# Kernel optimization log

Hardware: AMD Instinct MI355X
Metric: run time of the kernel (lower is better)

## Reference

```python
import jax, jax.numpy as jnp
import numpy as np

N, E, EDGES, G = 4096, 256, 131072, 64
H, DH = 4, 64  # MHA heads, head dim


def _ln(x, g, b, eps=1e-5):
    m = jnp.mean(x, -1, keepdims=True)
    v = jnp.var(x, -1, keepdims=True)
    return g * (x - m) * jax.lax.rsqrt(v + eps) + b


def setup_inputs() -> dict:
    key = jax.random.key(0)
    ks = jax.random.split(key, 40)
    i = iter(range(40))
    def rn(shape, s=1.0):
        return jax.random.normal(ks[next(i)], shape, jnp.float32) * s
    w = lambda shape: rn(shape, 0.02)
    inp = {
        "node_hidden": rn((N, E)),
        "edge_hidden": rn((EDGES, E)),
        "pos": rn((N, 3)),
        # GINEConv MLP: Lin(E,2E) -> LN -> ReLU -> Dropout -> Lin(2E,E)
        "gine_w1": w((E, 2 * E)), "gine_b1": jnp.zeros((2 * E,)),
        "gine_ln_g": jnp.ones((2 * E,)), "gine_ln_b": jnp.zeros((2 * E,)),
        "gine_w2": w((2 * E, E)), "gine_b2": jnp.zeros((E,)),
        "norm1_g": jnp.ones((E,)), "norm1_b": jnp.zeros((E,)),
        # DirectionalMessagePassing params
        "dir_w": w((3, E)), "dir_b": jnp.zeros((E,)),
        "msg_w": w((E, E)), "msg_b": jnp.zeros((E,)),
        # MultiheadAttention
        "wq": w((E, E)), "bq": jnp.zeros((E,)),
        "wk": w((E, E)), "bk": jnp.zeros((E,)),
        "wv": w((E, E)), "bv": jnp.zeros((E,)),
        "wo": w((E, E)), "bo": jnp.zeros((E,)),
        # gate
        "gate_w": w((2 * E, E)), "gate_b": jnp.zeros((E,)),
        "norm2_g": jnp.ones((E,)), "norm2_b": jnp.zeros((E,)),
        # GraphNorm affine
        "gn_g": jnp.ones((E,)), "gn_b": jnp.zeros((E,)),
        # int inputs
        "edge_index": jax.random.randint(ks[next(i)], (2, EDGES), 0, N, jnp.int64 if jax.config.jax_enable_x64 else jnp.int32),
        "node_id": jnp.sort(jax.random.randint(ks[next(i)], (N,), 0, G)),
        "edge_id": jax.random.randint(ks[next(i)], (EDGES,), 0, G),
    }
    return inp


def reference(node_hidden, edge_hidden, pos,
              gine_w1, gine_b1, gine_ln_g, gine_ln_b, gine_w2, gine_b2,
              norm1_g, norm1_b, dir_w, dir_b, msg_w, msg_b,
              wq, bq, wk, bk, wv, bv, wo, bo,
              gate_w, gate_b, norm2_g, norm2_b, gn_g, gn_b,
              edge_index, node_id, edge_id):
    src, dst = edge_index[0], edge_index[1]
    identity = node_hidden

    # --- GINEConv: out = MLP(x + sum_j relu(x_j + e_ij)), eps=0 ---
    msg = jax.nn.relu(node_hidden[src] + edge_hidden)           # [EDGES, E]
    agg = jax.ops.segment_sum(msg, dst, num_segments=N)         # [N, E]
    h = node_hidden + agg
    h = jax.nn.relu(_ln(h @ gine_w1 + gine_b1, gine_ln_g, gine_ln_b))
    gnn_out = _ln(h @ gine_w2 + gine_b2, norm1_g, norm1_b)      # norm1

    # --- DirectionalMessagePassing over unit edge directions ---
    vec = pos[dst] - pos[src]                                   # [EDGES, 3]
    vec = vec / (jnp.linalg.norm(vec, axis=-1, keepdims=True) + 1e-8)
    dfeat = vec @ dir_w + dir_b                                 # [EDGES, E]
    smsg = gnn_out[src] * dfeat
    sagg = jax.ops.segment_sum(smsg, dst, num_segments=N)
    spatial_out = sagg @ msg_w + msg_b                          # [N, E]

    # --- MHA: q = gnn_out, k = v = spatial_out (seq = nodes, batch=1) ---
    q = (gnn_out @ wq + bq).reshape(N, H, DH)
    k = (spatial_out @ wk + bk).reshape(N, H, DH)
    v = (spatial_out @ wv + bv).reshape(N, H, DH)
    scores = jnp.einsum("nhd,mhd->hnm", q, k) / np.sqrt(DH)
    attn = jax.nn.softmax(scores, axis=-1)
    fused = jnp.einsum("hnm,mhd->nhd", attn, v).reshape(N, E) @ wo + bo

    # --- gated residual blend + norm2 ---
    gate = jax.nn.sigmoid(jnp.concatenate([fused, identity], -1) @ gate_w + gate_b)
    out = gate * fused + (1.0 - gate) * identity
    out = _ln(out, norm2_g, norm2_b)

    # --- GraphNorm: per-graph mean/var over nodes (segment stats) ---
    counts = jax.ops.segment_sum(jnp.ones((N, 1), out.dtype), node_id, num_segments=G)
    mean = jax.ops.segment_sum(out, node_id, num_segments=G) / counts
    cen = out - mean[node_id]
    var = jax.ops.segment_sum(cen * cen, node_id, num_segments=G) / counts
    out = gn_g * cen * jax.lax.rsqrt(var[node_id] + 1e-5) + gn_b

    # last_act = True; dropout is eval-mode identity
    return jax.nn.relu(out)
```

## Files before the change

### kernel.cpp

```cpp
#include <hip/hip_runtime.h>
#include <hip/hip_bf16.h>

#define N_NODES 4096
#define E_DIM   256
#define N_EDGES 131072
#define N_GRAPHS 64
#define H_HEADS 4
#define DH      64
#define SPLIT   4

typedef unsigned short u16;
typedef __attribute__((ext_vector_type(8))) short bf16x8;
typedef __attribute__((ext_vector_type(4))) float f32x4;

__device__ __forceinline__ float u2f(u16 u) {
    union { unsigned int i; float f; } c; c.i = ((unsigned int)u) << 16; return c.f;
}
__device__ __forceinline__ u16 f2bu(float f) {
    __hip_bfloat16 h = __float2bfloat16(f);
    return *reinterpret_cast<u16*>(&h);
}
__device__ __forceinline__ float ldv(const void* p, size_t i, int f32) {
    return f32 ? ((const float*)p)[i] : u2f(((const u16*)p)[i]);
}
__device__ __forceinline__ float4 ldv4(const void* p, size_t i, int f32) {
    if (f32) return *(const float4*)((const float*)p + i);
    ushort4 u = *(const ushort4*)((const u16*)p + i);
    return make_float4(u2f(u.x), u2f(u.y), u2f(u.z), u2f(u.w));
}
__device__ __forceinline__ int ldi(const int* p, int i, int i64) {
    return i64 ? p[2 * i] : p[i];
}

__global__ void k_detect(const u16* __restrict__ ones_raw, const int* __restrict__ ei_raw,
                         int* __restrict__ flags) {
    flags[0] = (ones_raw[0] == 0) ? 1 : 0;
    flags[1] = (ei_raw[1] == 0 && ei_raw[3] == 0 && ei_raw[5] == 0 && ei_raw[7] == 0) ? 1 : 0;
}

__global__ void k_cvt(const void* __restrict__ s, float* __restrict__ d, int n,
                      const int* __restrict__ flags) {
    int i = blockIdx.x * 256 + threadIdx.x;
    if (i < n) d[i] = ldv(s, i, flags[0]);
}

struct SmDesc { const void* src; float* dst; int n; };
struct SmTable { SmDesc d[19]; };
__global__ __launch_bounds__(256) void k_cvts(SmTable tb, const int* __restrict__ flags) {
    int ti = blockIdx.x / 48;
    int off = (blockIdx.x % 48) * 256 + threadIdx.x;
    SmDesc e = tb.d[ti];
    if (off < e.n) e.dst[off] = ldv(e.src, off, flags[0]);
}

struct WtDesc { const void* src; u16* dst; int K; int N; int base; };
struct WtTable { WtDesc d[8]; };
__global__ __launch_bounds__(256) void k_cvtw(WtTable tb, const int* __restrict__ flags) {
    __shared__ u16 tile[64][68];
    int b = blockIdx.x;
    int i = 0;
    while (i < 7 && b >= tb.d[i + 1].base) i++;
    WtDesc e = tb.d[i];
    int tl = b - e.base;
    int ntn = e.N >> 6;
    int kt = tl / ntn, nt = tl % ntn;
    int t = threadIdx.x, r = t >> 2, c0 = (t & 3) * 16;
    int f32 = flags[0];
#pragma unroll
    for (int j = 0; j < 16; j++)
        tile[r][c0 + j] = f2bu(ldv(e.src, (size_t)(kt * 64 + r) * e.N + nt * 64 + c0 + j, f32));
    __syncthreads();
#pragma unroll
    for (int j = 0; j < 16; j++)
        e.dst[(size_t)(nt * 64 + r) * e.K + kt * 64 + c0 + j] = tile[c0 + j][r];
}

__global__ __launch_bounds__(256) void k_mgemm(const float* __restrict__ A0, const float* __restrict__ A1,
                                               int K0, int Ktot, const u16* __restrict__ BT,
                                               const float* __restrict__ bias, void* __restrict__ C,
                                               int Nc, int outbf) {
    __shared__ u16 As[64 * 64];
    __shared__ u16 Bs[64 * 64];
    int t = threadIdx.x;
    int wv = t >> 6, l = t & 63, lg = l >> 4, lc = l & 15;
    int wm = wv >> 1, wn = wv & 1;
    int m0 = blockIdx.y * 64, n0 = blockIdx.x * 64;
    f32x4 acc[2][2] = {};
    int sr = t >> 2, sc = (t & 3) * 16;
    int sw = (sr & 7) << 3;

    for (int k0 = 0; k0 < Ktot; k0 += 64) {
        const float* Ap = (k0 < K0) ? (A0 + (size_t)(m0 + sr) * K0 + k0 + sc)
                                    : (A1 + (size_t)(m0 + sr) * (Ktot - K0) + (k0 - K0) + sc);
#pragma unroll
        for (int j = 0; j < 2; j++) {
            float4 f0 = *(const float4*)(Ap + j * 8);
            float4 f1 = *(const float4*)(Ap + j * 8 + 4);
            bf16x8 bv;
            bv[0] = (short)f2bu(f0.x); bv[1] = (short)f2bu(f0.y);
            bv[2] = (short)f2bu(f0.z); bv[3] = (short)f2bu(f0.w);
            bv[4] = (short)f2bu(f1.x); bv[5] = (short)f2bu(f1.y);
            bv[6] = (short)f2bu(f1.z); bv[7] = (short)f2bu(f1.w);
            *(bf16x8*)&As[(sr * 64 + sc + j * 8) ^ sw] = bv;
        }
        const u16* Bp = BT + (size_t)(n0 + sr) * Ktot + k0 + sc;
        *(bf16x8*)&Bs[(sr * 64 + sc) ^ sw]     = *(const bf16x8*)Bp;
        *(bf16x8*)&Bs[(sr * 64 + sc + 8) ^ sw] = *(const bf16x8*)(Bp + 8);
        __syncthreads();
#pragma unroll
        for (int ks = 0; ks < 2; ks++) {
            bf16x8 af[2], bfr[2];
#pragma unroll
            for (int mi = 0; mi < 2; mi++) {
                int row = wm * 32 + mi * 16 + lc;
                af[mi] = *(const bf16x8*)&As[(row * 64 + ks * 32 + lg * 8) ^ ((row & 7) << 3)];
            }
#pragma unroll
            for (int ni = 0; ni < 2; ni++) {
                int col = wn * 32 + ni * 16 + lc;
                bfr[ni] = *(const bf16x8*)&Bs[(col * 64 + ks * 32 + lg * 8) ^ ((col & 7) << 3)];
            }
#pragma unroll
            for (int mi = 0; mi < 2; mi++)
#pragma unroll
                for (int ni = 0; ni < 2; ni++)
                    acc[mi][ni] = __builtin_amdgcn_mfma_f32_16x16x32_bf16(af[mi], bfr[ni], acc[mi][ni], 0, 0, 0);
        }
        __syncthreads();
    }
#pragma unroll
    for (int mi = 0; mi < 2; mi++)
#pragma unroll
        for (int ni = 0; ni < 2; ni++) {
            int col = n0 + wn * 32 + ni * 16 + lc;
            float bb = bias ? bias[col] : 0.f;
#pragma unroll
            for (int r = 0; r < 4; r++) {
                int row = m0 + wm * 32 + mi * 16 + lg * 4 + r;
                float v = acc[mi][ni][r] + bb;
                if (outbf) ((u16*)C)[(size_t)row * Nc + col] = f2bu(v);
                else       ((float*)C)[(size_t)row * Nc + col] = v;
            }
        }
}

__global__ __launch_bounds__(256) void k_transV(const u16* __restrict__ KVh, u16* __restrict__ VT) {
    __shared__ u16 tile[64][72];
    int n0 = blockIdx.x * 64, h = blockIdx.y, t = threadIdx.x;
    int r = t >> 2, c0 = (t & 3) * 16;
    const u16* src = &KVh[(size_t)(n0 + r) * 512 + 256 + h * DH + c0];
    *(bf16x8*)&tile[r][c0]     = *(const bf16x8*)src;
    *(bf16x8*)&tile[r][c0 + 8] = *(const bf16x8*)(src + 8);
    __syncthreads();
    u16* dst = &VT[((size_t)h * DH + r) * N_NODES + n0 + c0];
#pragma unroll
    for (int j = 0; j < 16; j++) dst[j] = tile[c0 + j][r];
}

__global__ __launch_bounds__(256) void k_attn(const u16* __restrict__ Qh, const u16* __restrict__ KVh,
                                              const u16* __restrict__ VT, u16* __restrict__ part) {
    __shared__ u16 K_lds[64 * 64];
    __shared__ u16 V_lds[64 * 64];
    __shared__ u16 P_lds[4][16 * 64];
    int t = threadIdx.x;
    int wv = t >> 6, l = t & 63;
    int lg = l >> 4, lc = l & 15;
    int h = blockIdx.y, c = blockIdx.z;
    int q0 = blockIdx.x * 64 + wv * 16;

    bf16x8 qf[2];
#pragma unroll
    for (int kk = 0; kk < 2; kk++)
        qf[kk] = *(const bf16x8*)&Qh[(size_t)(q0 + lc) * E_DIM + h * DH + kk * 32 + lg * 8];

    f32x4 oacc[4] = {};
    float mrow[4], lrow[4];
#pragma unroll
    for (int r = 0; r < 4; r++) { mrow[r] = -1e30f; lrow[r] = 0.f; }

    int lr = t >> 2, lc16 = (t & 3) * 16;

    for (int kv0 = c * (N_NODES / SPLIT); kv0 < (c + 1) * (N_NODES / SPLIT); kv0 += 64) {
        __syncthreads();
        {
            int base = lr * 64 + lc16;
            int sw = (lr & 7) << 3;
            const u16* kp = &KVh[(size_t)(kv0 + lr) * 512 + h * DH + lc16];
            *(bf16x8*)&K_lds[(base) ^ sw]     = *(const bf16x8*)kp;
            *(bf16x8*)&K_lds[(base + 8) ^ sw] = *(const bf16x8*)(kp + 8);
            const u16* vp = &VT[((size_t)h * DH + lr) * N_NODES + kv0 + lc16];
            *(bf16x8*)&V_lds[(base) ^ sw]     = *(const bf16x8*)vp;
            *(bf16x8*)&V_lds[(base + 8) ^ sw] = *(const bf16x8*)(vp + 8);
        }
        __syncthreads();

        f32x4 s[4];
#pragma unroll
        for (int n = 0; n < 4; n++) {
            f32x4 a = {};
#pragma unroll
            for (int kk = 0; kk < 2; kk++) {
                int row = n * 16 + lc;
                bf16x8 b = *(const bf16x8*)&K_lds[(row * 64 + kk * 32 + lg * 8) ^ ((row & 7) << 3)];
                a = __builtin_amdgcn_mfma_f32_16x16x32_bf16(qf[kk], b, a, 0, 0, 0);
            }
            s[n] = a;
        }
        float tm[4];
#pragma unroll
        for (int r = 0; r < 4; r++) {
#pragma unroll
            for (int n = 0; n < 4; n++) s[n][r] *= 0.125f;
            tm[r] = fmaxf(fmaxf(s[0][r], s[1][r]), fmaxf(s[2][r], s[3][r]));
        }
#pragma unroll
        for (int msk = 1; msk < 16; msk <<= 1)
#pragma unroll
            for (int r = 0; r < 4; r++) tm[r] = fmaxf(tm[r], __shfl_xor(tm[r], msk));

        float p[4][4], psum[4];
#pragma unroll
        for (int r = 0; r < 4; r++) {
            float nm = fmaxf(mrow[r], tm[r]);
            float alpha = __expf(mrow[r] - nm);
            lrow[r] *= alpha;
#pragma unroll
            for (int n = 0; n < 4; n++) oacc[n][r] *= alpha;
            float ps = 0.f;
#pragma unroll
            for (int n = 0; n < 4; n++) { p[n][r] = __expf(s[n][r] - nm); ps += p[n][r]; }
            psum[r] = ps;
            mrow[r] = nm;
        }
#pragma unroll
        for (int msk = 1; msk < 16; msk <<= 1)
#pragma unroll
            for (int r = 0; r < 4; r++) psum[r] += __shfl_xor(psum[r], msk);
#pragma unroll
        for (int r = 0; r < 4; r++) lrow[r] += psum[r];

#pragma unroll
        for (int r = 0; r < 4; r++) {
            int q = lg * 4 + r;
            int sw = (q & 7) << 3;
#pragma unroll
            for (int n = 0; n < 4; n++)
                P_lds[wv][(q * 64 + n * 16 + lc) ^ sw] = f2bu(p[n][r]);
        }
#pragma unroll
        for (int kc = 0; kc < 2; kc++) {
            bf16x8 a = *(const bf16x8*)&P_lds[wv][(lc * 64 + kc * 32 + lg * 8) ^ ((lc & 7) << 3)];
#pragma unroll
            for (int n = 0; n < 4; n++) {
                int row = n * 16 + lc;
                bf16x8 b = *(const bf16x8*)&V_lds[(row * 64 + kc * 32 + lg * 8) ^ ((row & 7) << 3)];
                oacc[n] = __builtin_amdgcn_mfma_f32_16x16x32_bf16(a, b, oacc[n], 0, 0, 0);
            }
        }
    }

#pragma unroll
    for (int r = 0; r < 4; r++) {
        u16* pp = part + ((size_t)(c * H_HEADS + h) * N_NODES + q0 + lg * 4 + r) * 72;
#pragma unroll
        for (int n = 0; n < 4; n++) pp[n * 16 + lc] = f2bu(oacc[n][r]);
        if (lc == 0) { *(float*)(pp + 64) = mrow[r]; *(float*)(pp + 66) = lrow[r]; }
    }
}

__global__ __launch_bounds__(256) void k_combine(const u16* __restrict__ part, float* __restrict__ attno) {
    int n = blockIdx.x, t = threadIdx.x;
    int h = t >> 6, d = t & 63;
    float M = -1e30f;
#pragma unroll
    for (int c = 0; c < SPLIT; c++)
        M = fmaxf(M, *(const float*)(part + ((size_t)(c * H_HEADS + h) * N_NODES + n) * 72 + 64));
    float L = 0.f, o = 0.f;
#pragma unroll
    for (int c = 0; c < SPLIT; c++) {
        const u16* pp = part + ((size_t)(c * H_HEADS + h) * N_NODES + n) * 72;
        float w = __expf(*(const float*)(pp + 64) - M);
        L = fmaf(*(const float*)(pp + 66), w, L);
        o = fmaf(u2f(pp[d]), w, o);
    }
    attno[(size_t)n * E_DIM + h * DH + d] = o / L;
}

__device__ __forceinline__ void block_red2(float& a, float& b, float* sbuf) {
#pragma unroll
    for (int o = 32; o > 0; o >>= 1) { a += __shfl_down(a, o); b += __shfl_down(b, o); }
    int w = threadIdx.x >> 6;
    if ((threadIdx.x & 63) == 0) { sbuf[w] = a; sbuf[4 + w] = b; }
    __syncthreads();
    a = sbuf[0] + sbuf[1] + sbuf[2] + sbuf[3];
    b = sbuf[4] + sbuf[5] + sbuf[6] + sbuf[7];
    __syncthreads();
}

__global__ void k_count(const int* __restrict__ ei, int* __restrict__ count,
                        const int* __restrict__ flags) {
    int e = blockIdx.x * 256 + threadIdx.x;
    int i64 = flags[1];
    int d = i64 ? ei[2 * (N_EDGES + e)] : ei[N_EDGES + e];
    atomicAdd(&count[d], 1);
}

__global__ __launch_bounds__(1024) void k_scan(const int* __restrict__ count,
                                               int* __restrict__ offs, int* __restrict__ cursor) {
    __shared__ int s[1024];
    int t = threadIdx.x;
    int c0 = count[t * 4 + 0], c1 = count[t * 4 + 1], c2 = count[t * 4 + 2], c3 = count[t * 4 + 3];
    int tot = c0 + c1 + c2 + c3;
    s[t] = tot; __syncthreads();
    for (int o = 1; o < 1024; o <<= 1) {
        int v = (t >= o) ? s[t - o] : 0;
        __syncthreads();
        s[t] += v;
        __syncthreads();
    }
    int base = (t > 0) ? s[t - 1] : 0;
    int o0 = base, o1 = base + c0, o2 = o1 + c1, o3 = o2 + c2;
    offs[t * 4 + 0] = o0; offs[t * 4 + 1] = o1; offs[t * 4 + 2] = o2; offs[t * 4 + 3] = o3;
    cursor[t * 4 + 0] = o0; cursor[t * 4 + 1] = o1; cursor[t * 4 + 2] = o2; cursor[t * 4 + 3] = o3;
    if (t == 1023) offs[4096] = s[1023];
}

__global__ void k_scatter(const int* __restrict__ ei, int* __restrict__ cursor,
                          int* __restrict__ elist, const int* __restrict__ flags) {
    int e = blockIdx.x * 256 + threadIdx.x;
    int i64 = flags[1];
    int d = i64 ? ei[2 * (N_EDGES + e)] : ei[N_EDGES + e];
    int p = atomicAdd(&cursor[d], 1);
    elist[p] = e;
}

__global__ __launch_bounds__(256) void k_gine_agg(const float* __restrict__ xf, const void* __restrict__ eh,
                                                  const int* __restrict__ ei, const int* __restrict__ offs,
                                                  const int* __restrict__ elist, const int* __restrict__ flags,
                                                  float* __restrict__ hout) {
    int wv = threadIdx.x >> 6, ld = threadIdx.x & 63;
    int n = blockIdx.x * 4 + wv;
    int f32 = flags[0], i64 = flags[1];
    int cc = ld * 4;
    float4 acc = *(const float4*)&xf[(size_t)n * E_DIM + cc];
    int i0 = offs[n], i1 = offs[n + 1];
    int i = i0;
    for (; i + 2 <= i1; i += 2) {
        int e0 = elist[i], e1 = elist[i + 1];
        int s0 = ldi(ei, e0, i64), s1 = ldi(ei, e1, i64);
        float4 a0 = ldv4(eh, (size_t)e0 * E_DIM + cc, f32);
        float4 x0 = *(const float4*)&xf[(size_t)s0 * E_DIM + cc];
        float4 a1 = ldv4(eh, (size_t)e1 * E_DIM + cc, f32);
        float4 x1 = *(const float4*)&xf[(size_t)s1 * E_DIM + cc];
        acc.x += fmaxf(x0.x + a0.x, 0.f) + fmaxf(x1.x + a1.x, 0.f);
        acc.y += fmaxf(x0.y + a0.y, 0.f) + fmaxf(x1.y + a1.y, 0.f);
        acc.z += fmaxf(x0.z + a0.z, 0.f) + fmaxf(x1.z + a1.z, 0.f);
        acc.w += fmaxf(x0.w + a0.w, 0.f) + fmaxf(x1.w + a1.w, 0.f);
    }
    if (i < i1) {
        int e0 = elist[i];
        int s0 = ldi(ei, e0, i64);
        float4 a0 = ldv4(eh, (size_t)e0 * E_DIM + cc, f32);
        float4 x0 = *(const float4*)&xf[(size_t)s0 * E_DIM + cc];
        acc.x += fmaxf(x0.x + a0.x, 0.f);
        acc.y += fmaxf(x0.y + a0.y, 0.f);
        acc.z += fmaxf(x0.z + a0.z, 0.f);
        acc.w += fmaxf(x0.w + a0.w, 0.f);
    }
    *(float4*)&hout[(size_t)n * E_DIM + cc] = acc;
}

template <int W>
__global__ __launch_bounds__(256) void k_ln(float* __restrict__ X, const float* __restrict__ g,
                                            const float* __restrict__ b, int relu) {
    __shared__ float sbuf[8];
    constexpr int PE = W / 256;
    int n = blockIdx.x, t = threadIdx.x;
    float* row = X + (size_t)n * W;
    float x[PE];
    float s = 0.f, s2 = 0.f;
#pragma unroll
    for (int i = 0; i < PE; i++) { x[i] = row[t + i * 256]; s += x[i]; s2 += x[i] * x[i]; }
    block_red2(s, s2, sbuf);
    float mean = s / W;
    float var = fmaxf(s2 / W - mean * mean, 0.f);
    float rstd = rsqrtf(var + 1e-5f);
#pragma unroll
    for (int i = 0; i < PE; i++) {
        int c = t + i * 256;
        float y = g[c] * (x[i] - mean) * rstd + b[c];
        if (relu) y = fmaxf(y, 0.f);
        row[c] = y;
    }
}

__global__ __launch_bounds__(256) void k_dir(const float* __restrict__ posf, const int* __restrict__ ei,
                                             const int* __restrict__ offs, const int* __restrict__ elist,
                                             const int* __restrict__ flags,
                                             const float* __restrict__ gnn, const float* __restrict__ dw,
                                             const float* __restrict__ db, float* __restrict__ sagg) {
    int wv = threadIdx.x >> 6, ld = threadIdx.x & 63;
    int n = blockIdx.x * 4 + wv;
    int i64 = flags[1];
    int cc = ld * 4;
    float4 w0 = *(const float4*)&dw[cc];
    float4 w1 = *(const float4*)&dw[256 + cc];
    float4 w2 = *(const float4*)&dw[512 + cc];
    float4 bb = *(const float4*)&db[cc];
    float px = posf[n * 3 + 0], py = posf[n * 3 + 1], pz = posf[n * 3 + 2];
    float4 acc = {0.f, 0.f, 0.f, 0.f};
    int i0 = offs[n], i1 = offs[n + 1];
    int i = i0;
    for (; i + 2 <= i1; i += 2) {
        int e0 = elist[i], e1 = elist[i + 1];
        int s0 = ldi(ei, e0, i64), s1 = ldi(ei, e1, i64);
        float q0x = posf[s0 * 3 + 0], q0y = posf[s0 * 3 + 1], q0z = posf[s0 * 3 + 2];
        float q1x = posf[s1 * 3 + 0], q1y = posf[s1 * 3 + 1], q1z = posf[s1 * 3 + 2];
        float4 g0 = *(const float4*)&gnn[(size_t)s0 * E_DIM + cc];
        float4 g1 = *(const float4*)&gnn[(size_t)s1 * E_DIM + cc];
        float vx0 = px - q0x, vy0 = py - q0y, vz0 = pz - q0z;
        float vx1 = px - q1x, vy1 = py - q1y, vz1 = pz - q1z;
        float rn0 = 1.f / (sqrtf(vx0 * vx0 + vy0 * vy0 + vz0 * vz0) + 1e-8f);
        float rn1 = 1.f / (sqrtf(vx1 * vx1 + vy1 * vy1 + vz1 * vz1) + 1e-8f);
        acc.x = fmaf(g0.x, bb.x + (vx0 * w0.x + vy0 * w1.x + vz0 * w2.x) * rn0, acc.x);
        acc.y = fmaf(g0.y, bb.y + (vx0 * w0.y + vy0 * w1.y + vz0 * w2.y) * rn0, acc.y);
        acc.z = fmaf(g0.z, bb.z + (vx0 * w0.z + vy0 * w1.z + vz0 * w2.z) * rn0, acc.z);
        acc.w = fmaf(g0.w, bb.w + (vx0 * w0.w + vy0 * w1.w + vz0 * w2.w) * rn0, acc.w);
        acc.x = fmaf(g1.x, bb.x + (vx1 * w0.x + vy1 * w1.x + vz1 * w2.x) * rn1, acc.x);
        acc.y = fmaf(g1.y, bb.y + (vx1 * w0.y + vy1 * w1.y + vz1 * w2.y) * rn1, acc.y);
        acc.z = fmaf(g1.z, bb.z + (vx1 * w0.z + vy1 * w1.z + vz1 * w2.z) * rn1, acc.z);
        acc.w = fmaf(g1.w, bb.w + (vx1 * w0.w + vy1 * w1.w + vz1 * w2.w) * rn1, acc.w);
    }
    if (i < i1) {
        int e0 = elist[i];
        int s0 = ldi(ei, e0, i64);
        float q0x = posf[s0 * 3 + 0], q0y = posf[s0 * 3 + 1], q0z = posf[s0 * 3 + 2];
        float4 g0 = *(const float4*)&gnn[(size_t)s0 * E_DIM + cc];
        float vx0 = px - q0x, vy0 = py - q0y, vz0 = pz - q0z;
        float rn0 = 1.f / (sqrtf(vx0 * vx0 + vy0 * vy0 + vz0 * vz0) + 1e-8f);
        acc.x = fmaf(g0.x, bb.x + (vx0 * w0.x + vy0 * w1.x + vz0 * w2.x) * rn0, acc.x);
        acc.y = fmaf(g0.y, bb.y + (vx0 * w0.y + vy0 * w1.y + vz0 * w2.y) * rn0, acc.y);
        acc.z = fmaf(g0.z, bb.z + (vx0 * w0.z + vy0 * w1.z + vz0 * w2.z) * rn0, acc.z);
        acc.w = fmaf(g0.w, bb.w + (vx0 * w0.w + vy0 * w1.w + vz0 * w2.w) * rn0, acc.w);
    }
    *(float4*)&sagg[(size_t)n * E_DIM + cc] = acc;
}

__global__ __launch_bounds__(256) void k_gate_ln(const float* __restrict__ gl, const float* __restrict__ fused,
                                                 const float* __restrict__ xf, const float* __restrict__ g2,
                                                 const float* __restrict__ b2, float* __restrict__ out2) {
    __shared__ float sbuf[8];
    int n = blockIdx.x, t = threadIdx.x;
    float z = gl[(size_t)n * E_DIM + t];
    float gate = 1.f / (1.f + __expf(-z));
    float o = gate * fused[(size_t)n * E_DIM + t] + (1.f - gate) * xf[(size_t)n * E_DIM + t];
    float s = o, s2 = o * o;
    block_red2(s, s2, sbuf);
    float mean = s / E_DIM;
    float var = fmaxf(s2 / E_DIM - mean * mean, 0.f);
    float y = g2[t] * (o - mean) * rsqrtf(var + 1e-5f) + b2[t];
    out2[(size_t)n * E_DIM + t] = y;
}

__global__ void k_bounds(const int* __restrict__ nid, int* __restrict__ startg,
                         const int* __restrict__ flags) {
    int t = threadIdx.x;
    int i64 = flags[1];
    if (t <= N_GRAPHS) {
        int lo = 0, hi = N_NODES;
        while (lo < hi) { int mid = (lo + hi) >> 1; if (ldi(nid, mid, i64) < t) lo = mid + 1; else hi = mid; }
        startg[t] = lo;
    }
}

__global__ __launch_bounds__(256) void k_gnstats(const int* __restrict__ startg, const float* __restrict__ out2,
                                                 float* __restrict__ gnm, float* __restrict__ gnr) {
    int g = blockIdx.x, t = threadIdx.x;
    int a = startg[g], bnd = startg[g + 1];
    int cnt = bnd - a;
    float s = 0.f, s2 = 0.f;
    for (int n = a; n < bnd; n++) {
        float x = out2[(size_t)n * E_DIM + t];
        s += x; s2 = fmaf(x, x, s2);
    }
    float inv = cnt ? 1.f / (float)cnt : 0.f;
    float mean = s * inv;
    float var = fmaxf(s2 * inv - mean * mean, 0.f);
    gnm[g * E_DIM + t] = mean;
    gnr[g * E_DIM + t] = rsqrtf(var + 1e-5f);
}

__global__ __launch_bounds__(256) void k_gnapply(const float* __restrict__ out2, const int* __restrict__ nid,
                                                 const float* __restrict__ gnm, const float* __restrict__ gnr,
                                                 const float* __restrict__ gg, const float* __restrict__ gb,
                                                 const int* __restrict__ flags, void* __restrict__ out) {
    int n = blockIdx.x, t = threadIdx.x;
    int g = ldi(nid, n, flags[1]);
    float y = gg[t] * (out2[(size_t)n * E_DIM + t] - gnm[g * E_DIM + t]) * gnr[g * E_DIM + t] + gb[t];
    y = fmaxf(y, 0.f);
    size_t idx = (size_t)n * E_DIM + t;
    if (flags[0]) ((float*)out)[idx] = y;
    else ((__hip_bfloat16*)out)[idx] = __float2bfloat16(y);
}

extern "C" void kernel_launch(void* const* d_in, const int* in_sizes, int n_in,
                              void* d_out, int out_size, void* d_ws, size_t ws_size,
                              hipStream_t stream) {
    const void* x_r    = d_in[0];
    const void* eh_r   = d_in[1];
    const void* pos_r  = d_in[2];
    const void* w1_r   = d_in[3];
    const void* b1_r   = d_in[4];
    const void* glng_r = d_in[5];
    const void* glnb_r = d_in[6];
    const void* w2_r   = d_in[7];
    const void* b2_r   = d_in[8];
    const void* n1g_r  = d_in[9];
    const void* n1b_r  = d_in[10];
    const void* dirw_r = d_in[11];
    const void* dirb_r = d_in[12];
    const void* msgw_r = d_in[13];
    const void* msgb_r = d_in[14];
    const void* wq_r   = d_in[15];
    const void* bq_r   = d_in[16];
    const void* wk_r   = d_in[17];
    const void* bk_r   = d_in[18];
    const void* wv_r   = d_in[19];
    const void* bv_r   = d_in[20];
    const void* wo_r   = d_in[21];
    const void* bo_r   = d_in[22];
    const void* gw_r   = d_in[23];
    const void* gb_r   = d_in[24];
    const void* n2g_r  = d_in[25];
    const void* n2b_r  = d_in[26];
    const void* gng_r  = d_in[27];
    const void* gnb_r  = d_in[28];
    const int* ei      = (const int*)d_in[29];
    const int* nid     = (const int*)d_in[30];

    char* ws = (char*)d_ws;
    const size_t KB = 1 << 10, MB = 1 << 20;
    int*   flags  = (int*)(ws + 0);
    int*   count  = (int*)(ws + 16 * KB);
    int*   offs   = (int*)(ws + 32 * KB);
    int*   cursor = (int*)(ws + 64 * KB);
    int*   elist  = (int*)(ws + 128 * KB);

    float* posf   = (float*)(ws + 1 * MB);
    float* prm    = (float*)(ws + 1 * MB + 64 * KB);
    float* b1f   = prm + 0;
    float* glngf = prm + 512,  *glnbf = prm + 1024;
    float* b2f   = prm + 1536;
    float* n1gf  = prm + 1792, *n1bf  = prm + 2048;
    float* dirwf = prm + 2304;
    float* dirbf = prm + 3072, *msgbf = prm + 3328;
    float* bqf   = prm + 3584, *bkf   = prm + 3840, *bvf = prm + 4096, *bof = prm + 4352;
    float* gbf   = prm + 4608;
    float* n2gf  = prm + 4864, *n2bf  = prm + 5120;
    float* gngf  = prm + 5376, *gnbf  = prm + 5632;

    u16* w1t   = (u16*)(ws + 2 * MB);
    u16* w2t   = (u16*)(ws + 2 * MB + 256 * KB);
    u16* msgwt = (u16*)(ws + 2 * MB + 512 * KB);
    u16* wqt   = (u16*)(ws + 2 * MB + 640 * KB);
    u16* wkvt  = (u16*)(ws + 2 * MB + 768 * KB);
    u16* wot   = (u16*)(ws + 3 * MB + 0 * KB);
    u16* gwt   = (u16*)(ws + 3 * MB + 128 * KB);

    float* xf     = (float*)(ws + 5 * MB);
    float* hbuf   = (float*)(ws + 9 * MB);
    float* T1     = (float*)(ws + 13 * MB);
    float* gnn    = (float*)(ws + 21 * MB);
    float* sagg   = (float*)(ws + 25 * MB);
    float* spat   = (float*)(ws + 29 * MB);
    u16*   Qh     = (u16*)(ws + 9 * MB);
    u16*   KVh    = (u16*)(ws + 13 * MB);
    u16*   VT     = (u16*)(ws + 17 * MB);
    u16*   part   = (u16*)(ws + 19 * MB);
    float* attno  = (float*)(ws + 13 * MB);
    float* fused  = (float*)(ws + 29 * MB);
    float* gatel  = (float*)(ws + 19 * MB);
    float* out2   = (float*)(ws + 23 * MB);
    float* gnm    = (float*)(ws + 29 * MB);
    float* gnr    = (float*)(ws + 29 * MB + 64 * KB);
    int*   startg = (int*)(ws + 29 * MB + 128 * KB);

    k_detect<<<1, 1, 0, stream>>>((const u16*)glng_r, ei, flags);

    k_cvt<<<(N_NODES * E_DIM + 255) / 256, 256, 0, stream>>>(x_r, xf, N_NODES * E_DIM, flags);

    SmTable st;
    {
        int i = 0;
        auto add = [&](const void* s, float* d, int n) { st.d[i].src = s; st.d[i].dst = d; st.d[i].n = n; i++; };
        add(pos_r, posf, N_NODES * 3);
        add(b1_r, b1f, 512); add(glng_r, glngf, 512); add(glnb_r, glnbf, 512);
        add(b2_r, b2f, 256); add(n1g_r, n1gf, 256); add(n1b_r, n1bf, 256);
        add(dirw_r, dirwf, 768); add(dirb_r, dirbf, 256); add(msgb_r, msgbf, 256);
        add(bq_r, bqf, 256); add(bk_r, bkf, 256); add(bv_r, bvf, 256); add(bo_r, bof, 256);
        add(gb_r, gbf, 256); add(n2g_r, n2gf, 256); add(n2b_r, n2bf, 256);
        add(gng_r, gngf, 256); add(gnb_r, gnbf, 256);
    }
    k_cvts<<<19 * 48, 256, 0, stream>>>(st, flags);

    WtTable wt;
    {
        int i = 0, base = 0;
        auto add = [&](const void* s, u16* d, int K, int N) {
            wt.d[i].src = s; wt.d[i].dst = d; wt.d[i].K = K; wt.d[i].N = N; wt.d[i].base = base;
            base += (K / 64) * (N / 64); i++;
        };
        add(w1_r, w1t, 256, 512);
        add(w2_r, w2t, 512, 256);
        add(msgw_r, msgwt, 256, 256);
        add(wq_r, wqt, 256, 256);
        add(wk_r, wkvt, 256, 256);
        add(wv_r, wkvt + 256 * 256, 256, 256);
        add(wo_r, wot, 256, 256);
        add(gw_r, gwt, 512, 256);
        k_cvtw<<<base, 256, 0, stream>>>(wt, flags);
    }

    hipMemsetAsync(count, 0, N_NODES * sizeof(int), stream);
    k_count<<<N_EDGES / 256, 256, 0, stream>>>(ei, count, flags);
    k_scan<<<1, 1024, 0, stream>>>(count, offs, cursor);
    k_scatter<<<N_EDGES / 256, 256, 0, stream>>>(ei, cursor, elist, flags);

    k_gine_agg<<<N_NODES / 4, 256, 0, stream>>>(xf, eh_r, ei, offs, elist, flags, hbuf);
    k_mgemm<<<dim3(8, 64), 256, 0, stream>>>(hbuf, nullptr, 256, 256, w1t, b1f, T1, 512, 0);
    k_ln<512><<<N_NODES, 256, 0, stream>>>(T1, glngf, glnbf, 1);
    k_mgemm<<<dim3(4, 64), 256, 0, stream>>>(T1, nullptr, 512, 512, w2t, b2f, gnn, 256, 0);
    k_ln<256><<<N_NODES, 256, 0, stream>>>(gnn, n1gf, n1bf, 0);

    k_dir<<<N_NODES / 4, 256, 0, stream>>>(posf, ei, offs, elist, flags, gnn, dirwf, dirbf, sagg);
    k_mgemm<<<dim3(4, 64), 256, 0, stream>>>(sagg, nullptr, 256, 256, msgwt, msgbf, spat, 256, 0);

    k_mgemm<<<dim3(4, 64), 256, 0, stream>>>(gnn, nullptr, 256, 256, wqt, bqf, Qh, 256, 1);
    k_mgemm<<<dim3(8, 64), 256, 0, stream>>>(spat, nullptr, 256, 256, wkvt, bkf, KVh, 512, 1);
    k_transV<<<dim3(64, 4), 256, 0, stream>>>(KVh, VT);

    k_attn<<<dim3(N_NODES / 64, H_HEADS, SPLIT), 256, 0, stream>>>(Qh, KVh, VT, part);
    k_combine<<<N_NODES, 256, 0, stream>>>(part, attno);
    k_mgemm<<<dim3(4, 64), 256, 0, stream>>>(attno, nullptr, 256, 256, wot, bof, fused, 256, 0);

    k_mgemm<<<dim3(4, 64), 256, 0, stream>>>(fused, xf, 256, 512, gwt, gbf, gatel, 256, 0);
    k_gate_ln<<<N_NODES, 256, 0, stream>>>(gatel, fused, xf, n2gf, n2bf, out2);

    k_bounds<<<1, 128, 0, stream>>>(nid, startg, flags);
    k_gnstats<<<N_GRAPHS, 256, 0, stream>>>(startg, out2, gnm, gnr);
    k_gnapply<<<N_NODES, 256, 0, stream>>>(out2, nid, gnm, gnr, gngf, gnbf, flags, d_out);
}
```

Baseline: 295.6 us.

## Fold msg projection into K/V weights and fuse QKV GEMM with V transpose

Precomputes msg_w·[wk|wv] and the matching biases so spatial_out is never materialised, then computes Q, K and V in a single GEMM over [gnn|sagg] that also writes the transposed V directly. It also doubles the attention KV split, writes the attention output as bf16 so the out-projection reads bf16, replaces the 1024-thread scan with a wave-shuffle scan, unrolls the GINE gather by four, and folds the graph-bound search into the stats kernel. This removes several kernel launches and intermediate buffers. The price is extra per-call weight-prep GEMMs, and multiplying the weights together before rounding to bf16 changes the rounding behaviour.

Measured after the change: 292.2 us. Within noise of the previous version (-1.1%).

```diff
diff --git a/kernel.cpp b/kernel.cpp
--- a/kernel.cpp
+++ b/kernel.cpp
@@ -7,7 +7,7 @@
 #define N_GRAPHS 64
 #define H_HEADS 4
 #define DH      64
-#define SPLIT   4
+#define SPLIT   8
 
 typedef unsigned short u16;
 typedef __attribute__((ext_vector_type(8))) short bf16x8;
@@ -42,6 +42,17 @@
                       const int* __restrict__ flags) {
     int i = blockIdx.x * 256 + threadIdx.x;
     if (i < n) d[i] = ldv(s, i, flags[0]);
+}
+
+__global__ void k_cvtb(const void* __restrict__ s, u16* __restrict__ d, int n4,
+                       const int* __restrict__ flags) {
+    int i = blockIdx.x * 256 + threadIdx.x;
+    if (i < n4) {
+        float4 v = ldv4(s, (size_t)i * 4, flags[0]);
+        ushort4 o;
+        o.x = f2bu(v.x); o.y = f2bu(v.y); o.z = f2bu(v.z); o.w = f2bu(v.w);
+        ((ushort4*)d)[i] = o;
+    }
 }
 
 struct SmDesc { const void* src; float* dst; int n; };
@@ -75,10 +86,24 @@
         e.dst[(size_t)(nt * 64 + r) * e.K + kt * 64 + c0 + j] = tile[c0 + j][r];
 }
 
-__global__ __launch_bounds__(256) void k_mgemm(const float* __restrict__ A0, const float* __restrict__ A1,
+__global__ __launch_bounds__(256) void k_biasfold(const float* __restrict__ bq, const float* __restrict__ bk,
+                                                  const float* __restrict__ bv, const float* __restrict__ msgb,
+                                                  const u16* __restrict__ wkvt, float* __restrict__ bqkv) {
+    int t = blockIdx.x * 256 + threadIdx.x;
+    if (t < 256) { bqkv[t] = bq[t]; return; }
+    int c = t - 256;
+    float s = (c < 256) ? bk[c] : bv[c - 256];
+    const u16* row = wkvt + (size_t)c * 256;
+    float acc = 0.f;
+    for (int k = 0; k < 256; k++) acc = fmaf(msgb[k], u2f(row[k]), acc);
+    bqkv[256 + c] = s + acc;
+}
+
+__global__ __launch_bounds__(256) void k_mgemm(const void* __restrict__ A0, const void* __restrict__ A1,
                                                int K0, int Ktot, const u16* __restrict__ BT,
                                                const float* __restrict__ bias, void* __restrict__ C,
-                                               int Nc, int outbf) {
+                                               int Nc, int outbf, int abf, int mode,
+                                               u16* __restrict__ vt) {
     __shared__ u16 As[64 * 64];
     __shared__ u16 Bs[64 * 64];
     int t = threadIdx.x;
@@ -90,18 +115,27 @@
     int sw = (sr & 7) << 3;
 
     for (int k0 = 0; k0 < Ktot; k0 += 64) {
-        const float* Ap = (k0 < K0) ? (A0 + (size_t)(m0 + sr) * K0 + k0 + sc)
-                                    : (A1 + (size_t)(m0 + sr) * (Ktot - K0) + (k0 - K0) + sc);
-#pragma unroll
-        for (int j = 0; j < 2; j++) {
-            float4 f0 = *(const float4*)(Ap + j * 8);
-            float4 f1 = *(const float4*)(Ap + j * 8 + 4);
-            bf16x8 bv;
-            bv[0] = (short)f2bu(f0.x); bv[1] = (short)f2bu(f0.y);
-            bv[2] = (short)f2bu(f0.z); bv[3] = (short)f2bu(f0.w);
-            bv[4] = (short)f2bu(f1.x); bv[5] = (short)f2bu(f1.y);
-            bv[6] = (short)f2bu(f1.z); bv[7] = (short)f2bu(f1.w);
-            *(bf16x8*)&As[(sr * 64 + sc + j * 8) ^ sw] = bv;
+        const void* Abase; int astride, kof;
+        if (mode == 1) { Abase = (n0 < K0) ? A0 : A1; astride = Ktot; kof = k0; }
+        else if (k0 < K0) { Abase = A0; astride = K0; kof = k0; }
+        else { Abase = A1; astride = Ktot - K0; kof = k0 - K0; }
+        if (abf) {
+            const u16* Ap = (const u16*)Abase + (size_t)(m0 + sr) * astride + kof + sc;
+            *(bf16x8*)&As[(sr * 64 + sc) ^ sw]     = *(const bf16x8*)Ap;
+            *(bf16x8*)&As[(sr * 64 + sc + 8) ^ sw] = *(const bf16x8*)(Ap + 8);
+        } else {
+            const float* Ap = (const float*)Abase + (size_t)(m0 + sr) * astride + kof + sc;
+#pragma unroll
+            for (int j = 0; j < 2; j++) {
+                float4 f0 = *(const float4*)(Ap + j * 8);
+                float4 f1 = *(const float4*)(Ap + j * 8 + 4);
+                bf16x8 bv;
+                bv[0] = (short)f2bu(f0.x); bv[1] = (short)f2bu(f0.y);
+                bv[2] = (short)f2bu(f0.z); bv[3] = (short)f2bu(f0.w);
+                bv[4] = (short)f2bu(f1.x); bv[5] = (short)f2bu(f1.y);
+                bv[6] = (short)f2bu(f1.z); bv[7] = (short)f2bu(f1.w);
+                *(bf16x8*)&As[(sr * 64 + sc + j * 8) ^ sw] = bv;
+            }
         }
         const u16* Bp = BT + (size_t)(n0 + sr) * Ktot + k0 + sc;
         *(bf16x8*)&Bs[(sr * 64 + sc) ^ sw]     = *(const bf16x8*)Bp;
@@ -138,27 +172,16 @@
             for (int r = 0; r < 4; r++) {
                 int row = m0 + wm * 32 + mi * 16 + lg * 4 + r;
                 float v = acc[mi][ni][r] + bb;
-                if (outbf) ((u16*)C)[(size_t)row * Nc + col] = f2bu(v);
+                u16 hb = f2bu(v);
+                if (outbf) ((u16*)C)[(size_t)row * Nc + col] = hb;
                 else       ((float*)C)[(size_t)row * Nc + col] = v;
+                if (vt && col >= 512) vt[(size_t)(col - 512) * N_NODES + row] = hb;
             }
         }
 }
 
-__global__ __launch_bounds__(256) void k_transV(const u16* __restrict__ KVh, u16* __restrict__ VT) {
-    __shared__ u16 tile[64][72];
-    int n0 = blockIdx.x * 64, h = blockIdx.y, t = threadIdx.x;
-    int r = t >> 2, c0 = (t & 3) * 16;
-    const u16* src = &KVh[(size_t)(n0 + r) * 512 + 256 + h * DH + c0];
-    *(bf16x8*)&tile[r][c0]     = *(const bf16x8*)src;
-    *(bf16x8*)&tile[r][c0 + 8] = *(const bf16x8*)(src + 8);
-    __syncthreads();
-    u16* dst = &VT[((size_t)h * DH + r) * N_NODES + n0 + c0];
-#pragma unroll
-    for (int j = 0; j < 16; j++) dst[j] = tile[c0 + j][r];
-}
-
-__global__ __launch_bounds__(256) void k_attn(const u16* __restrict__ Qh, const u16* __restrict__ KVh,
-                                              const u16* __restrict__ VT, u16* __restrict__ part) {
+__global__ __launch_bounds__(256) void k_attn(const u16* __restrict__ QKV, const u16* __restrict__ VT,
+                                              u16* __restrict__ part) {
     __shared__ u16 K_lds[64 * 64];
     __shared__ u16 V_lds[64 * 64];
     __shared__ u16 P_lds[4][16 * 64];
@@ -171,7 +194,7 @@
     bf16x8 qf[2];
 #pragma unroll
     for (int kk = 0; kk < 2; kk++)
-        qf[kk] = *(const bf16x8*)&Qh[(size_t)(q0 + lc) * E_DIM + h * DH + kk * 32 + lg * 8];
+        qf[kk] = *(const bf16x8*)&QKV[(size_t)(q0 + lc) * 768 + h * DH + kk * 32 + lg * 8];
 
     f32x4 oacc[4] = {};
     float mrow[4], lrow[4];
@@ -185,7 +208,7 @@
         {
             int base = lr * 64 + lc16;
             int sw = (lr & 7) << 3;
-            const u16* kp = &KVh[(size_t)(kv0 + lr) * 512 + h * DH + lc16];
+            const u16* kp = &QKV[(size_t)(kv0 + lr) * 768 + 256 + h * DH + lc16];
             *(bf16x8*)&K_lds[(base) ^ sw]     = *(const bf16x8*)kp;
             *(bf16x8*)&K_lds[(base + 8) ^ sw] = *(const bf16x8*)(kp + 8);
             const u16* vp = &VT[((size_t)h * DH + lr) * N_NODES + kv0 + lc16];
@@ -268,7 +291,7 @@
     }
 }
 
-__global__ __launch_bounds__(256) void k_combine(const u16* __restrict__ part, float* __restrict__ attno) {
+__global__ __launch_bounds__(256) void k_combine(const u16* __restrict__ part, u16* __restrict__ attnoh) {
     int n = blockIdx.x, t = threadIdx.x;
     int h = t >> 6, d = t & 63;
     float M = -1e30f;
@@ -283,7 +306,7 @@
         L = fmaf(*(const float*)(pp + 66), w, L);
         o = fmaf(u2f(pp[d]), w, o);
     }
-    attno[(size_t)n * E_DIM + h * DH + d] = o / L;
+    attnoh[(size_t)n * E_DIM + h * DH + d] = f2bu(o / L);
 }
 
 __device__ __forceinline__ void block_red2(float& a, float& b, float* sbuf) {
@@ -307,22 +330,27 @@
 
 __global__ __launch_bounds__(1024) void k_scan(const int* __restrict__ count,
                                                int* __restrict__ offs, int* __restrict__ cursor) {
-    __shared__ int s[1024];
-    int t = threadIdx.x;
+    __shared__ int wsum[16];
+    int t = threadIdx.x, lane = t & 63, wid = t >> 6;
     int c0 = count[t * 4 + 0], c1 = count[t * 4 + 1], c2 = count[t * 4 + 2], c3 = count[t * 4 + 3];
     int tot = c0 + c1 + c2 + c3;
-    s[t] = tot; __syncthreads();
-    for (int o = 1; o < 1024; o <<= 1) {
-        int v = (t >= o) ? s[t - o] : 0;
-        __syncthreads();
-        s[t] += v;
-        __syncthreads();
-    }
-    int base = (t > 0) ? s[t - 1] : 0;
+    int inc = tot;
+#pragma unroll
+    for (int o = 1; o < 64; o <<= 1) { int v = __shfl_up(inc, o); if (lane >= o) inc += v; }
+    if (lane == 63) wsum[wid] = inc;
+    __syncthreads();
+    if (t < 16) {
+        int v = wsum[t];
+#pragma unroll
+        for (int o = 1; o < 16; o <<= 1) { int u = __shfl_up(v, o); if (t >= o) v += u; }
+        wsum[t] = v;
+    }
+    __syncthreads();
+    int base = (wid ? wsum[wid - 1] : 0) + inc - tot;
     int o0 = base, o1 = base + c0, o2 = o1 + c1, o3 = o2 + c2;
     offs[t * 4 + 0] = o0; offs[t * 4 + 1] = o1; offs[t * 4 + 2] = o2; offs[t * 4 + 3] = o3;
     cursor[t * 4 + 0] = o0; cursor[t * 4 + 1] = o1; cursor[t * 4 + 2] = o2; cursor[t * 4 + 3] = o3;
-    if (t == 1023) offs[4096] = s[1023];
+    if (t == 1023) offs[4096] = wsum[15];
 }
 
 __global__ void k_scatter(const int* __restrict__ ei, int* __restrict__ cursor,
@@ -345,19 +373,26 @@
     float4 acc = *(const float4*)&xf[(size_t)n * E_DIM + cc];
     int i0 = offs[n], i1 = offs[n + 1];
     int i = i0;
-    for (; i + 2 <= i1; i += 2) {
-        int e0 = elist[i], e1 = elist[i + 1];
-        int s0 = ldi(ei, e0, i64), s1 = ldi(ei, e1, i64);
-        float4 a0 = ldv4(eh, (size_t)e0 * E_DIM + cc, f32);
-        float4 x0 = *(const float4*)&xf[(size_t)s0 * E_DIM + cc];
-        float4 a1 = ldv4(eh, (size_t)e1 * E_DIM + cc, f32);
-        float4 x1 = *(const float4*)&xf[(size_t)s1 * E_DIM + cc];
-        acc.x += fmaxf(x0.x + a0.x, 0.f) + fmaxf(x1.x + a1.x, 0.f);
-        acc.y += fmaxf(x0.y + a0.y, 0.f) + fmaxf(x1.y + a1.y, 0.f);
-        acc.z += fmaxf(x0.z + a0.z, 0.f) + fmaxf(x1.z + a1.z, 0.f);
-        acc.w += fmaxf(x0.w + a0.w, 0.f) + fmaxf(x1.w + a1.w, 0.f);
-    }
-    if (i < i1) {
+    for (; i + 4 <= i1; i += 4) {
+        int e[4], s[4];
+#pragma unroll
+        for (int j = 0; j < 4; j++) e[j] = elist[i + j];
+#pragma unroll
+        for (int j = 0; j < 4; j++) s[j] = ldi(ei, e[j], i64);
+        float4 a[4], x[4];
+#pragma unroll
+        for (int j = 0; j < 4; j++) a[j] = ldv4(eh, (size_t)e[j] * E_DIM + cc, f32);
+#pragma unroll
+        for (int j = 0; j < 4; j++) x[j] = *(const float4*)&xf[(size_t)s[j] * E_DIM + cc];
+#pragma unroll
+        for (int j = 0; j < 4; j++) {
+            acc.x += fmaxf(x[j].x + a[j].x, 0.f);
+            acc.y += fmaxf(x[j].y + a[j].y, 0.f);
+            acc.z += fmaxf(x[j].z + a[j].z, 0.f);
+            acc.w += fmaxf(x[j].w + a[j].w, 0.f);
+        }
+    }
+    for (; i < i1; i++) {
         int e0 = elist[i];
         int s0 = ldi(ei, e0, i64);
         float4 a0 = ldv4(eh, (size_t)e0 * E_DIM + cc, f32);
@@ -462,21 +497,18 @@
     out2[(size_t)n * E_DIM + t] = y;
 }
 
-__global__ void k_bounds(const int* __restrict__ nid, int* __restrict__ startg,
-                         const int* __restrict__ flags) {
-    int t = threadIdx.x;
-    int i64 = flags[1];
-    if (t <= N_GRAPHS) {
-        int lo = 0, hi = N_NODES;
-        while (lo < hi) { int mid = (lo + hi) >> 1; if (ldi(nid, mid, i64) < t) lo = mid + 1; else hi = mid; }
-        startg[t] = lo;
-    }
-}
-
-__global__ __launch_bounds__(256) void k_gnstats(const int* __restrict__ startg, const float* __restrict__ out2,
+__device__ __forceinline__ int lbound(const int* __restrict__ nid, int v, int i64) {
+    int lo = 0, hi = N_NODES;
+    while (lo < hi) { int mid = (lo + hi) >> 1; if (ldi(nid, mid, i64) < v) lo = mid + 1; else hi = mid; }
+    return lo;
+}
+
+__global__ __launch_bounds__(256) void k_gnstats(const int* __restrict__ nid, const int* __restrict__ flags,
+                                                 const float* __restrict__ out2,
                                                  float* __restrict__ gnm, float* __restrict__ gnr) {
     int g = blockIdx.x, t = threadIdx.x;
-    int a = startg[g], bnd = startg[g + 1];
+    int i64 = flags[1];
+    int a = lbound(nid, g, i64), bnd = lbound(nid, g + 1, i64);
     int cnt = bnd - a;
     float s = 0.f, s2 = 0.f;
     for (int n = a; n < bnd; n++) {
@@ -559,31 +591,29 @@
     float* n2gf  = prm + 4864, *n2bf  = prm + 5120;
     float* gngf  = prm + 5376, *gnbf  = prm + 5632;
 
-    u16* w1t   = (u16*)(ws + 2 * MB);
-    u16* w2t   = (u16*)(ws + 2 * MB + 256 * KB);
-    u16* msgwt = (u16*)(ws + 2 * MB + 512 * KB);
-    u16* wqt   = (u16*)(ws + 2 * MB + 640 * KB);
-    u16* wkvt  = (u16*)(ws + 2 * MB + 768 * KB);
-    u16* wot   = (u16*)(ws + 3 * MB + 0 * KB);
-    u16* gwt   = (u16*)(ws + 3 * MB + 128 * KB);
+    u16* w1t    = (u16*)(ws + 2 * MB);
+    u16* w2t    = (u16*)(ws + 2 * MB + 256 * KB);
+    u16* wot    = (u16*)(ws + 2 * MB + 512 * KB);
+    u16* gwt    = (u16*)(ws + 2 * MB + 640 * KB);
+    u16* wqkvt  = (u16*)(ws + 3 * MB);
+    u16* wkvt   = (u16*)(ws + 3 * MB + 384 * KB);
+    u16* msgwb  = (u16*)(ws + 3 * MB + 640 * KB);
+    float* bqkvf = (float*)(ws + 3 * MB + 768 * KB);
 
     float* xf     = (float*)(ws + 5 * MB);
     float* hbuf   = (float*)(ws + 9 * MB);
     float* T1     = (float*)(ws + 13 * MB);
     float* gnn    = (float*)(ws + 21 * MB);
     float* sagg   = (float*)(ws + 25 * MB);
-    float* spat   = (float*)(ws + 29 * MB);
-    u16*   Qh     = (u16*)(ws + 9 * MB);
-    u16*   KVh    = (u16*)(ws + 13 * MB);
-    u16*   VT     = (u16*)(ws + 17 * MB);
-    u16*   part   = (u16*)(ws + 19 * MB);
-    float* attno  = (float*)(ws + 13 * MB);
-    float* fused  = (float*)(ws + 29 * MB);
-    float* gatel  = (float*)(ws + 19 * MB);
-    float* out2   = (float*)(ws + 23 * MB);
-    float* gnm    = (float*)(ws + 29 * MB);
-    float* gnr    = (float*)(ws + 29 * MB + 64 * KB);
-    int*   startg = (int*)(ws + 29 * MB + 128 * KB);
+    u16*   QKVh   = (u16*)(ws + 29 * MB);
+    u16*   VT     = (u16*)(ws + 35 * MB);
+    u16*   part   = (u16*)(ws + 37 * MB);
+    u16*   attnoh = (u16*)(ws + 9 * MB);
+    float* fused  = (float*)(ws + 13 * MB);
+    float* gatel  = (float*)(ws + 17 * MB);
+    float* out2   = (float*)(ws + 21 * MB);
+    float* gnm    = (float*)(ws + 25 * MB);
+    float* gnr    = (float*)(ws + 25 * MB + 64 * KB);
 
     k_detect<<<1, 1, 0, stream>>>((const u16*)glng_r, ei, flags);
 
@@ -612,14 +642,18 @@
         };
         add(w1_r, w1t, 256, 512);
         add(w2_r, w2t, 512, 256);
-        add(msgw_r, msgwt, 256, 256);
-        add(wq_r, wqt, 256, 256);
+        add(wq_r, wqkvt, 256, 256);
         add(wk_r, wkvt, 256, 256);
         add(wv_r, wkvt + 256 * 256, 256, 256);
         add(wo_r, wot, 256, 256);
         add(gw_r, gwt, 512, 256);
+        wt.d[7].base = 0x7fffffff;
         k_cvtw<<<base, 256, 0, stream>>>(wt, flags);
     }
+    k_cvtb<<<64, 256, 0, stream>>>(msgw_r, msgwb, 256 * 256 / 4, flags);
+    k_mgemm<<<dim3(4, 8), 256, 0, stream>>>(wkvt, nullptr, 256, 256, msgwb, nullptr,
+                                            wqkvt + 256 * 256, 256, 1, 1, 0, nullptr);
+    k_biasfold<<<3, 256, 0, stream>>>(bqf, bkf, bvf, msgbf, wkvt, bqkvf);
 
     hipMemsetAsync(count, 0, N_NODES * sizeof(int), stream);
     k_count<<<N_EDGES / 256, 256, 0, stream>>>(ei, count, flags);
@@ -627,26 +661,22 @@
     k_scatter<<<N_EDGES / 256, 256, 0, stream>>>(ei, cursor, elist, flags);
 
     k_gine_agg<<<N_NODES / 4, 256, 0, stream>>>(xf, eh_r, ei, offs, elist, flags, hbuf);
-    k_mgemm<<<dim3(8, 64), 256, 0, stream>>>(hbuf, nullptr, 256, 256, w1t, b1f, T1, 512, 0);
+    k_mgemm<<<dim3(8, 64), 256, 0, stream>>>(hbuf, nullptr, 256, 256, w1t, b1f, T1, 512, 0, 0, 0, nullptr);
     k_ln<512><<<N_NODES, 256, 0, stream>>>(T1, glngf, glnbf, 1);
-    k_mgemm<<<dim3(4, 64), 256, 0, stream>>>(T1, nullptr, 512, 512, w2t, b2f, gnn, 256, 0);
+    k_mgemm<<<dim3(4, 64), 256, 0, stream>>>(T1, nullptr, 512, 512, w2t, b2f, gnn, 256, 0, 0, 0, nullptr);
     k_ln<256><<<N_NODES, 256, 0, stream>>>(gnn, n1gf, n1bf, 0);
 
     k_dir<<<N_NODES / 4, 256, 0, stream>>>(posf, ei, offs, elist, flags, gnn, dirwf, dirbf, sagg);
-    k_mgemm<<<dim3(4, 64), 256, 0, stream>>>(sagg, nullptr, 256, 256, msgwt, msgbf, spat, 256, 0);
-
-    k_mgemm<<<dim3(4, 64), 256, 0, stream>>>(gnn, nullptr, 256, 256, wqt, bqf, Qh, 256, 1);
-    k_mgemm<<<dim3(8, 64), 256, 0, stream>>>(spat, nullptr, 256, 256, wkvt, bkf, KVh, 512, 1);
-    k_transV<<<dim3(64, 4), 256, 0, stream>>>(KVh, VT);
-
-    k_attn<<<dim3(N_NODES / 64, H_HEADS, SPLIT), 256, 0, stream>>>(Qh, KVh, VT, part);
-    k_combine<<<N_NODES, 256, 0, stream>>>(part, attno);
-    k_mgemm<<<dim3(4, 64), 256, 0, stream>>>(attno, nullptr, 256, 256, wot, bof, fused, 256, 0);
-
-    k_mgemm<<<dim3(4, 64), 256, 0, stream>>>(fused, xf, 256, 512, gwt, gbf, gatel, 256, 0);
+
+    k_mgemm<<<dim3(12, 64), 256, 0, stream>>>(gnn, sagg, 256, 256, wqkvt, bqkvf, QKVh, 768, 1, 0, 1, VT);
+
+    k_attn<<<dim3(N_NODES / 64, H_HEADS, SPLIT), 256, 0, stream>>>(QKVh, VT, part);
+    k_combine<<<N_NODES, 256, 0, stream>>>(part, attnoh);
+    k_mgemm<<<dim3(4, 64), 256, 0, stream>>>(attnoh, nullptr, 256, 256, wot, bof, fused, 256, 0, 1, 0, nullptr);
+
+    k_mgemm<<<dim3(4, 64), 256, 0, stream>>>(fused, xf, 256, 512, gwt, gbf, gatel, 256, 0, 0, 0, nullptr);
     k_gate_ln<<<N_NODES, 256, 0, stream>>>(gatel, fused, xf, n2gf, n2bf, out2);
 
-    k_bounds<<<1, 128, 0, stream>>>(nid, startg, flags);
-    k_gnstats<<<N_GRAPHS, 256, 0, stream>>>(startg, out2, gnm, gnr);
+    k_gnstats<<<N_GRAPHS, 256, 0, stream>>>(nid, flags, out2, gnm, gnr);
     k_gnapply<<<N_NODES, 256, 0, stream>>>(out2, nid, gnm, gnr, gngf, gnbf, flags, d_out);
 }
```
